# Performance work log

Hardware: AMD Instinct MI355X
Metric: run time of the kernel (lower is better)

The kernel has to match this reference:

```python
import jax, jax.numpy as jnp
import numpy as np
import math

B, S, D, H = 2, 2048, 1024, 16
DK = D // H
EPS = 1e-5


def setup_inputs() -> dict:
    key = jax.random.key(0)
    ks = jax.random.split(key, 16)
    s = 0.02
    inp = {
        "query": jax.random.normal(ks[0], (B, S, D), jnp.float32),
        "key": jax.random.normal(ks[1], (B, S, D), jnp.float32),
        "value": jax.random.normal(ks[2], (B, S, D), jnp.float32),
        "complexity": jax.random.uniform(ks[3], (B, S), jnp.float32),
        "mask": jnp.broadcast_to(jnp.tril(jnp.ones((S, S), bool))[None, None], (B, 1, S, S)),
        "wq": jax.random.normal(ks[4], (D, D), jnp.float32) * s,
        "bq": jnp.zeros((D,), jnp.float32),
        "wk": jax.random.normal(ks[5], (D, D), jnp.float32) * s,
        "bk": jnp.zeros((D,), jnp.float32),
        "wv": jax.random.normal(ks[6], (D, D), jnp.float32) * s,
        "bv": jnp.zeros((D,), jnp.float32),
        "wo": jax.random.normal(ks[7], (D, D), jnp.float32) * s,
        "bo": jnp.zeros((D,), jnp.float32),
        "ln_g": jnp.ones((D,), jnp.float32),
        "ln_b": jnp.zeros((D,), jnp.float32),
        "cpen": jnp.float32(1.0),
    }
    return inp


def reference(query, key, value, complexity, mask, wq, bq, wk, bk, wv, bv, wo, bo, ln_g, ln_b, cpen):
    # projections; torch Linear uses y = x @ W.T + b
    def proj(x, w, b):
        return (x @ w.T + b).reshape(B, S, H, DK).transpose(0, 2, 1, 3)  # [B,H,S,DK]

    Q = proj(query, wq, bq)
    K = proj(key, wk, bk)
    V = proj(value, wv, bv)

    scores = jnp.einsum("bhqd,bhkd->bhqk", Q, K) / math.sqrt(DK)
    # additive per-key-token complexity penalty broadcast over heads and queries
    scores = scores - cpen * complexity[:, None, None, :]
    scores = jnp.where(mask, scores, jnp.float32(-1e9))
    attn = jax.nn.softmax(scores, axis=-1)
    ctx = jnp.einsum("bhqk,bhkd->bhqd", attn, V)
    ctx = ctx.transpose(0, 2, 1, 3).reshape(B, S, D)
    out = ctx @ wo.T + bo
    x = out + query
    mu = jnp.mean(x, axis=-1, keepdims=True)
    var = jnp.mean(jnp.square(x - mu), axis=-1, keepdims=True)
    return (x - mu) * jax.lax.rsqrt(var + EPS) * ln_g + ln_b
```

## Files before the change

### kernel.cpp

```cpp
#include <hip/hip_runtime.h>

#define BB 2
#define SS 2048
#define DD 1024
#define HH 16
#define DKK 64
#define MROWS (BB*SS)
#define NEG_BIG (-30000.0f)

typedef unsigned short u16;
typedef unsigned int u32;
typedef __bf16 bf16x8 __attribute__((ext_vector_type(8)));
typedef float f32x4 __attribute__((ext_vector_type(4)));

__device__ __forceinline__ u16 f2bf(float f) {
    union { float f; u32 i; } w; w.f = f;
    u32 u = w.i;
    return (u16)((u + 0x7fffu + ((u >> 16) & 1u)) >> 16);
}
__device__ __forceinline__ float bf2f(u16 u) {
    union { u32 i; float f; } w; w.i = ((u32)u) << 16; return w.f;
}
__device__ __forceinline__ u32 pack2(float lo, float hi) {
    union { float f; u32 i; } a, b; a.f = lo; b.f = hi;
    return (a.i >> 16) | (b.i & 0xffff0000u);
}
__device__ __forceinline__ void gl2lds16(const u16* g, u16* l) {
    __builtin_amdgcn_global_load_lds(
        (const __attribute__((address_space(1))) void*)g,
        (__attribute__((address_space(3))) void*)l, 16, 0, 0);
}

__global__ __launch_bounds__(256)
void cvt_w(const float* __restrict__ w0, const float* __restrict__ w1,
           const float* __restrict__ w2, const float* __restrict__ w3,
           u16* __restrict__ dst)
{
    const float* srcs[4] = {w0, w1, w2, w3};
    const float* s = srcs[blockIdx.y];
    int i = (blockIdx.x * 256 + threadIdx.x) * 8;
    float4 a = *(const float4*)(s + i);
    float4 b = *(const float4*)(s + i + 4);
    uint4 o;
    o.x = pack2(a.x, a.y); o.y = pack2(a.z, a.w);
    o.z = pack2(b.x, b.y); o.w = pack2(b.z, b.w);
    *(uint4*)(dst + (size_t)blockIdx.y * DD * DD + i) = o;
}

__global__ __launch_bounds__(256)
void cvt_x(const float* __restrict__ s, u16* __restrict__ dst)
{
    int i = (blockIdx.x * 256 + threadIdx.x) * 8;
    float4 a = *(const float4*)(s + i);
    float4 b = *(const float4*)(s + i + 4);
    uint4 o;
    o.x = pack2(a.x, a.y); o.y = pack2(a.z, a.w);
    o.z = pack2(b.x, b.y); o.w = pack2(b.z, b.w);
    *(uint4*)(dst + i) = o;
}

__global__ __launch_bounds__(256)
void cvt_a3(const float* __restrict__ q, const float* __restrict__ k,
            const float* __restrict__ v, u16* __restrict__ qb,
            u16* __restrict__ kb, u16* __restrict__ vb)
{
    int y = blockIdx.y;
    const float* s = (y == 0) ? q : (y == 1) ? k : v;
    u16* d = (y == 0) ? qb : (y == 1) ? kb : vb;
    int i = (blockIdx.x * 256 + threadIdx.x) * 8;
    float4 a = *(const float4*)(s + i);
    float4 b = *(const float4*)(s + i + 4);
    uint4 o;
    o.x = pack2(a.x, a.y); o.y = pack2(a.z, a.w);
    o.z = pack2(b.x, b.y); o.w = pack2(b.z, b.w);
    *(uint4*)(d + i) = o;
}

__global__ __launch_bounds__(256, 2)
void qkv_gemm(const u16* __restrict__ qbf, const u16* __restrict__ kbf,
              const u16* __restrict__ vbf, const u16* __restrict__ wbf,
              const float* __restrict__ bq, const float* __restrict__ bk,
              const float* __restrict__ bv,
              u16* __restrict__ qh, u16* __restrict__ kh, u16* __restrict__ vt)
{
    __shared__ __align__(16) u16 smem[16384];
    u16* As = smem;
    u16* Bs = smem + 8192;
    const int K = 1024;
    int y = blockIdx.y;
    const u16* A = (y == 0) ? qbf : (y == 1) ? kbf : vbf;
    const u16* Wb = wbf + (size_t)y * DD * DD;
    const float* bias = (y == 0) ? bq : (y == 1) ? bk : bv;
    u16* out = (y == 0) ? qh : (y == 1) ? kh : vt;

    int tid  = threadIdx.x;
    int wave = tid >> 6, lane = tid & 63;
    int quad = lane >> 4, l16 = lane & 15;
    int bm = blockIdx.x >> 3;
    int bn = blockIdx.x & 7;
    int row0 = bm * 128, col0 = bn * 128;
    int wm = (wave >> 1) * 64, wn = (wave & 1) * 64;

    f32x4 acc[4][4] = {};

    for (int k0 = 0; k0 < K; k0 += 64) {
        __syncthreads();
        #pragma unroll
        for (int c = 0; c < 4; ++c) {
            int r0 = (c * 4 + wave) * 8;
            gl2lds16(A  + (size_t)(row0 + r0 + (lane >> 3)) * K + k0 + (lane & 7) * 8,
                     As + r0 * 64);
            gl2lds16(Wb + (size_t)(col0 + r0 + (lane >> 3)) * K + k0 + (lane & 7) * 8,
                     Bs + r0 * 64);
        }
        __syncthreads();
        #pragma unroll
        for (int kk = 0; kk < 2; ++kk) {
            bf16x8 af[4], bfv[4];
            #pragma unroll
            for (int i = 0; i < 4; ++i)
                af[i] = *(const bf16x8*)&As[(wm + i * 16 + l16) * 64 + kk * 32 + quad * 8];
            #pragma unroll
            for (int j = 0; j < 4; ++j)
                bfv[j] = *(const bf16x8*)&Bs[(wn + j * 16 + l16) * 64 + kk * 32 + quad * 8];
            #pragma unroll
            for (int i = 0; i < 4; ++i)
                #pragma unroll
                for (int j = 0; j < 4; ++j)
                    acc[i][j] = __builtin_amdgcn_mfma_f32_16x16x32_bf16(af[i], bfv[j], acc[i][j], 0, 0, 0);
        }
    }

    if (y == 2) {
        u16* Ct = smem;
        int b = row0 >> 11;
        int s0 = row0 & (SS - 1);
        #pragma unroll
        for (int p = 0; p < 2; ++p) {
            __syncthreads();
            if ((wave & 1) == p) {
                #pragma unroll
                for (int j = 0; j < 4; ++j) {
                    int dkl = j * 16 + l16;
                    float bvv = bias[col0 + p * 64 + dkl];
                    #pragma unroll
                    for (int i = 0; i < 4; ++i) {
                        uint2 pw;
                        pw.x = pack2(acc[i][j][0] + bvv, acc[i][j][1] + bvv);
                        pw.y = pack2(acc[i][j][2] + bvv, acc[i][j][3] + bvv);
                        *(uint2*)&Ct[dkl * 136 + wm + i * 16 + quad * 4] = pw;
                    }
                }
            }
            __syncthreads();
            int dkl = tid >> 2, seg = (tid & 3) * 32;
            int n = col0 + p * 64 + dkl;
            int h = n >> 6, dk = n & 63;
            u16* dst = out + (((size_t)(b * HH + h)) * DKK + dk) * SS + s0 + seg;
            #pragma unroll
            for (int u = 0; u < 4; ++u)
                *(uint4*)(dst + u * 8) = *(const uint4*)&Ct[dkl * 136 + seg + u * 8];
        }
        return;
    }

    #pragma unroll
    for (int j = 0; j < 4; ++j) {
        int n = col0 + wn + j * 16 + l16;
        float bvv = bias[n];
        #pragma unroll
        for (int i = 0; i < 4; ++i) {
            int rbase = row0 + wm + i * 16 + quad * 4;
            #pragma unroll
            for (int r = 0; r < 4; ++r) {
                int m = rbase + r;
                int b = m >> 11, s = m & (SS - 1);
                int h = n >> 6, dk = n & 63;
                out[(((size_t)(b * HH + h)) * SS + s) * DKK + dk] = f2bf(acc[i][j][r] + bvv);
            }
        }
    }
}

__global__ __launch_bounds__(256, 2)
void gemm_osk(const u16* __restrict__ A, const u16* __restrict__ Wb,
              const float* __restrict__ bias, float* __restrict__ P)
{
    __shared__ __align__(16) u16 smem[16384];
    u16* As = smem;
    u16* Bs = smem + 8192;
    const int K = 1024;
    int khalf = blockIdx.y;
    int tid  = threadIdx.x;
    int wave = tid >> 6, lane = tid & 63;
    int quad = lane >> 4, l16 = lane & 15;
    int bm = blockIdx.x >> 3;
    int bn = blockIdx.x & 7;
    int row0 = bm * 128, col0 = bn * 128;
    int wm = (wave >> 1) * 64, wn = (wave & 1) * 64;

    f32x4 acc[4][4] = {};

    for (int k0 = khalf * 512; k0 < khalf * 512 + 512; k0 += 64) {
        __syncthreads();
        #pragma unroll
        for (int c = 0; c < 4; ++c) {
            int r0 = (c * 4 + wave) * 8;
            gl2lds16(A  + (size_t)(row0 + r0 + (lane >> 3)) * K + k0 + (lane & 7) * 8,
                     As + r0 * 64);
            gl2lds16(Wb + (size_t)(col0 + r0 + (lane >> 3)) * K + k0 + (lane & 7) * 8,
                     Bs + r0 * 64);
        }
        __syncthreads();
        #pragma unroll
        for (int kk = 0; kk < 2; ++kk) {
            bf16x8 af[4], bfv[4];
            #pragma unroll
            for (int i = 0; i < 4; ++i)
                af[i] = *(const bf16x8*)&As[(wm + i * 16 + l16) * 64 + kk * 32 + quad * 8];
            #pragma unroll
            for (int j = 0; j < 4; ++j)
                bfv[j] = *(const bf16x8*)&Bs[(wn + j * 16 + l16) * 64 + kk * 32 + quad * 8];
            #pragma unroll
            for (int i = 0; i < 4; ++i)
                #pragma unroll
                for (int j = 0; j < 4; ++j)
                    acc[i][j] = __builtin_amdgcn_mfma_f32_16x16x32_bf16(af[i], bfv[j], acc[i][j], 0, 0, 0);
        }
    }

    float* Pd = P + (size_t)khalf * MROWS * DD;
    #pragma unroll
    for (int j = 0; j < 4; ++j) {
        int n = col0 + wn + j * 16 + l16;
        float bvv = (khalf == 0) ? bias[n] : 0.f;
        #pragma unroll
        for (int i = 0; i < 4; ++i) {
            int rbase = row0 + wm + i * 16 + quad * 4;
            #pragma unroll
            for (int r = 0; r < 4; ++r)
                Pd[(size_t)(rbase + r) * DD + n] = acc[i][j][r] + bvv;
        }
    }
}

template<int MODE>
__global__ __launch_bounds__(256, 2)
void gemm_nt(const u16* __restrict__ A, const u16* __restrict__ Wb,
             const float* __restrict__ bias, u16* __restrict__ out)
{
    __shared__ __align__(16) u16 smem[16384];
    u16* As = smem;
    u16* Bs = smem + 8192;
    const int K = 1024;
    int tid  = threadIdx.x;
    int wave = tid >> 6, lane = tid & 63;
    int quad = lane >> 4, l16 = lane & 15;
    int bm = blockIdx.x >> 3;
    int bn = blockIdx.x & 7;
    int row0 = bm * 128, col0 = bn * 128;
    int wm = (wave >> 1) * 64, wn = (wave & 1) * 64;

    f32x4 acc[4][4] = {};

    for (int k0 = 0; k0 < K; k0 += 64) {
        __syncthreads();
        #pragma unroll
        for (int c = 0; c < 4; ++c) {
            int r0 = (c * 4 + wave) * 8;
            gl2lds16(A  + (size_t)(row0 + r0 + (lane >> 3)) * K + k0 + (lane & 7) * 8,
                     As + r0 * 64);
            gl2lds16(Wb + (size_t)(col0 + r0 + (lane >> 3)) * K + k0 + (lane & 7) * 8,
                     Bs + r0 * 64);
        }
        __syncthreads();
        #pragma unroll
        for (int kk = 0; kk < 2; ++kk) {
            bf16x8 af[4], bfv[4];
            #pragma unroll
            for (int i = 0; i < 4; ++i)
                af[i] = *(const bf16x8*)&As[(wm + i * 16 + l16) * 64 + kk * 32 + quad * 8];
            #pragma unroll
            for (int j = 0; j < 4; ++j)
                bfv[j] = *(const bf16x8*)&Bs[(wn + j * 16 + l16) * 64 + kk * 32 + quad * 8];
            #pragma unroll
            for (int i = 0; i < 4; ++i)
                #pragma unroll
                for (int j = 0; j < 4; ++j)
                    acc[i][j] = __builtin_amdgcn_mfma_f32_16x16x32_bf16(af[i], bfv[j], acc[i][j], 0, 0, 0);
        }
    }

    if (MODE == 2) {
        u16* Ct = smem;
        int b = row0 >> 11;
        int s0 = row0 & (SS - 1);
        #pragma unroll
        for (int p = 0; p < 2; ++p) {
            __syncthreads();
            if ((wave & 1) == p) {
                #pragma unroll
                for (int j = 0; j < 4; ++j) {
                    int dkl = j * 16 + l16;
                    float bvv = bias[col0 + p * 64 + dkl];
                    #pragma unroll
                    for (int i = 0; i < 4; ++i) {
                        uint2 pw;
                        pw.x = pack2(acc[i][j][0] + bvv, acc[i][j][1] + bvv);
                        pw.y = pack2(acc[i][j][2] + bvv, acc[i][j][3] + bvv);
                        *(uint2*)&Ct[dkl * 136 + wm + i * 16 + quad * 4] = pw;
                    }
                }
            }
            __syncthreads();
            int dkl = tid >> 2, seg = (tid & 3) * 32;
            int n = col0 + p * 64 + dkl;
            int h = n >> 6, dk = n & 63;
            u16* dst = out + (((size_t)(b * HH + h)) * DKK + dk) * SS + s0 + seg;
            #pragma unroll
            for (int u = 0; u < 4; ++u)
                *(uint4*)(dst + u * 8) = *(const uint4*)&Ct[dkl * 136 + seg + u * 8];
        }
        return;
    }

    #pragma unroll
    for (int j = 0; j < 4; ++j) {
        int n = col0 + wn + j * 16 + l16;
        float bvv = bias[n];
        #pragma unroll
        for (int i = 0; i < 4; ++i) {
            int rbase = row0 + wm + i * 16 + quad * 4;
            #pragma unroll
            for (int r = 0; r < 4; ++r) {
                int m = rbase + r;
                float v = acc[i][j][r] + bvv;
                if (MODE == 0) {
                    int b = m >> 11, s = m & (SS - 1);
                    int h = n >> 6, dk = n & 63;
                    out[(((size_t)(b * HH + h)) * SS + s) * DKK + dk] = f2bf(v);
                } else {
                    out[(size_t)m * DD + n] = f2bf(v);
                }
            }
        }
    }
}

__global__ __launch_bounds__(256, 3)
void attn5(const u16* __restrict__ Qh, const u16* __restrict__ Kh,
           const u16* __restrict__ Vt, const float* __restrict__ comp,
           const float* __restrict__ cpen_p, u16* __restrict__ ctx)
{
    __shared__ __align__(16) u16 Kl[64 * 64];
    __shared__ __align__(16) u16 Vtl[64 * 64];
    __shared__ __align__(16) u16 Pb[4][16 * 72];

    int tid  = threadIdx.x;
    int wave = tid >> 6, lane = tid & 63;
    int quad = lane >> 4, l16 = lane & 15;
    int blk = blockIdx.x;
    int bh  = blk & 31;
    int qt  = 31 - (blk >> 5);
    int q0  = qt * 64;
    int b = bh >> 4, h = bh & 15;
    float cpen = cpen_p[0];

    const u16* Qb = Qh + (size_t)bh * SS * DKK;
    const u16* Kb = Kh + (size_t)bh * SS * DKK;
    const u16* Vb = Vt + (size_t)bh * DKK * SS;

    int myq = q0 + wave * 16 + l16;
    bf16x8 qf0 = *(const bf16x8*)&Qb[(size_t)myq * DKK + quad * 8];
    bf16x8 qf1 = *(const bf16x8*)&Qb[(size_t)myq * DKK + 32 + quad * 8];

    f32x4 o[4] = {};
    float m_i = NEG_BIG, l_i = 0.f;

    for (int kt = 0; kt <= qt; ++kt) {
        __syncthreads();
        if (wave < 2) {
            #pragma unroll
            for (int c = 0; c < 4; ++c) {
                int idx = wave * 4 + c;
                gl2lds16(Kb + (size_t)kt * 4096 + idx * 512 + lane * 8,
                         Kl + idx * 512);
            }
        } else {
            #pragma unroll
            for (int c = 0; c < 4; ++c) {
                int r0 = ((wave - 2) * 4 + c) * 8;
                gl2lds16(Vb + (size_t)(r0 + (lane >> 3)) * SS + kt * 64 + (lane & 7) * 8,
                         Vtl + r0 * 64);
            }
        }
        __syncthreads();

        f32x4 sc[4] = {};
        #pragma unroll
        for (int jj = 0; jj < 4; ++jj) {
            bf16x8 kf0 = *(const bf16x8*)&Kl[(jj * 16 + l16) * 64 + quad * 8];
            bf16x8 kf1 = *(const bf16x8*)&Kl[(jj * 16 + l16) * 64 + 32 + quad * 8];
            sc[jj] = __builtin_amdgcn_mfma_f32_16x16x32_bf16(kf0, qf0, sc[jj], 0, 0, 0);
            sc[jj] = __builtin_amdgcn_mfma_f32_16x16x32_bf16(kf1, qf1, sc[jj], 0, 0, 0);
        }
        bool diag = (kt == qt);
        #pragma unroll
        for (int jj = 0; jj < 4; ++jj) {
            f32x4 c4 = *(const f32x4*)&comp[b * SS + kt * 64 + jj * 16 + quad * 4];
            int kb0 = kt * 64 + jj * 16 + quad * 4;
            #pragma unroll
            for (int r = 0; r < 4; ++r) {
                float sv = sc[jj][r] * 0.125f - cpen * c4[r];
                if (diag && (kb0 + r > myq)) sv = NEG_BIG;
                sc[jj][r] = sv;
            }
        }
        float mx = NEG_BIG;
        #pragma unroll
        for (int jj = 0; jj < 4; ++jj)
            #pragma unroll
            for (int r = 0; r < 4; ++r) mx = fmaxf(mx, sc[jj][r]);
        mx = fmaxf(mx, __shfl_xor(mx, 16, 64));
        mx = fmaxf(mx, __shfl_xor(mx, 32, 64));
        float mnew = fmaxf(m_i, mx);
        float alpha = __expf(m_i - mnew);
        m_i = mnew;
        float ls = 0.f;
        #pragma unroll
        for (int jj = 0; jj < 4; ++jj)
            #pragma unroll
            for (int r = 0; r < 4; ++r) {
                float p = __expf(sc[jj][r] - mnew);
                sc[jj][r] = p;
                ls += p;
            }
        ls += __shfl_xor(ls, 16, 64);
        ls += __shfl_xor(ls, 32, 64);
        l_i = l_i * alpha + ls;
        #pragma unroll
        for (int jj = 0; jj < 4; ++jj)
            #pragma unroll
            for (int r = 0; r < 4; ++r) o[jj][r] *= alpha;

        #pragma unroll
        for (int jj = 0; jj < 4; ++jj) {
            uint2 pw;
            pw.x = pack2(sc[jj][0], sc[jj][1]);
            pw.y = pack2(sc[jj][2], sc[jj][3]);
            *(uint2*)&Pb[wave][l16 * 72 + jj * 16 + quad * 4] = pw;
        }
        #pragma unroll
        for (int kk = 0; kk < 2; ++kk) {
            bf16x8 pf = *(const bf16x8*)&Pb[wave][l16 * 72 + kk * 32 + quad * 8];
            #pragma unroll
            for (int jj = 0; jj < 4; ++jj) {
                bf16x8 vf = *(const bf16x8*)&Vtl[(jj * 16 + l16) * 64 + kk * 32 + quad * 8];
                o[jj] = __builtin_amdgcn_mfma_f32_16x16x32_bf16(vf, pf, o[jj], 0, 0, 0);
            }
        }
    }

    float inv = 1.f / l_i;
    #pragma unroll
    for (int jj = 0; jj < 4; ++jj) {
        uint2 ow;
        ow.x = pack2(o[jj][0] * inv, o[jj][1] * inv);
        ow.y = pack2(o[jj][2] * inv, o[jj][3] * inv);
        *(uint2*)&Pb[wave][l16 * 72 + jj * 16 + quad * 4] = ow;
    }
    int qq = lane >> 2;
    int dseg = (lane & 3) * 16;
    uint4 r0 = *(const uint4*)&Pb[wave][qq * 72 + dseg];
    uint4 r1 = *(const uint4*)&Pb[wave][qq * 72 + dseg + 8];
    u16* dst = ctx + ((size_t)(b * SS + q0 + wave * 16 + qq)) * DD + h * DKK + dseg;
    *(uint4*)dst = r0;
    *(uint4*)(dst + 8) = r1;
}

__global__ __launch_bounds__(256)
void ln_res(const u16* __restrict__ po, const float* __restrict__ query,
            const float* __restrict__ g, const float* __restrict__ bb,
            float* __restrict__ out)
{
    int row = blockIdx.x;
    int tid = threadIdx.x;
    int lane = tid & 63, wave = tid >> 6;
    size_t base = (size_t)row * DD + tid * 4;
    __align__(8) u16 tp[4];
    *(uint2*)tp = *(const uint2*)(po + base);
    float4 q4 = *(const float4*)(query + base);
    float x[4];
    x[0] = bf2f(tp[0]) + q4.x; x[1] = bf2f(tp[1]) + q4.y;
    x[2] = bf2f(tp[2]) + q4.z; x[3] = bf2f(tp[3]) + q4.w;
    float s1 = 0.f, s2 = 0.f;
    #pragma unroll
    for (int i = 0; i < 4; ++i) { s1 += x[i]; s2 += x[i] * x[i]; }
    #pragma unroll
    for (int off = 1; off < 64; off <<= 1) {
        s1 += __shfl_xor(s1, off, 64);
        s2 += __shfl_xor(s2, off, 64);
    }
    __shared__ float red1[4], red2[4];
    if (lane == 0) { red1[wave] = s1; red2[wave] = s2; }
    __syncthreads();
    float t1 = red1[0] + red1[1] + red1[2] + red1[3];
    float t2 = red2[0] + red2[1] + red2[2] + red2[3];
    float mean = t1 * (1.f / 1024.f);
    float var  = fmaxf(t2 * (1.f / 1024.f) - mean * mean, 0.f);
    float rstd = rsqrtf(var + 1e-5f);
    float4 g4 = *(const float4*)(g + tid * 4);
    float4 b4 = *(const float4*)(bb + tid * 4);
    float4 ov;
    ov.x = (x[0] - mean) * rstd * g4.x + b4.x;
    ov.y = (x[1] - mean) * rstd * g4.y + b4.y;
    ov.z = (x[2] - mean) * rstd * g4.z + b4.z;
    ov.w = (x[3] - mean) * rstd * g4.w + b4.w;
    *(float4*)(out + base) = ov;
}

__global__ __launch_bounds__(256)
void ln_res2(const float* __restrict__ p0, const float* __restrict__ p1,
             const float* __restrict__ query, const float* __restrict__ g,
             const float* __restrict__ bb, float* __restrict__ out)
{
    int row = blockIdx.x;
    int tid = threadIdx.x;
    int lane = tid & 63, wave = tid >> 6;
    size_t base = (size_t)row * DD + tid * 4;
    float4 a4 = *(const float4*)(p0 + base);
    float4 c4 = *(const float4*)(p1 + base);
    float4 q4 = *(const float4*)(query + base);
    float x[4];
    x[0] = a4.x + c4.x + q4.x; x[1] = a4.y + c4.y + q4.y;
    x[2] = a4.z + c4.z + q4.z; x[3] = a4.w + c4.w + q4.w;
    float s1 = 0.f, s2 = 0.f;
    #pragma unroll
    for (int i = 0; i < 4; ++i) { s1 += x[i]; s2 += x[i] * x[i]; }
    #pragma unroll
    for (int off = 1; off < 64; off <<= 1) {
        s1 += __shfl_xor(s1, off, 64);
        s2 += __shfl_xor(s2, off, 64);
    }
    __shared__ float red1[4], red2[4];
    if (lane == 0) { red1[wave] = s1; red2[wave] = s2; }
    __syncthreads();
    float t1 = red1[0] + red1[1] + red1[2] + red1[3];
    float t2 = red2[0] + red2[1] + red2[2] + red2[3];
    float mean = t1 * (1.f / 1024.f);
    float var  = fmaxf(t2 * (1.f / 1024.f) - mean * mean, 0.f);
    float rstd = rsqrtf(var + 1e-5f);
    float4 g4 = *(const float4*)(g + tid * 4);
    float4 b4 = *(const float4*)(bb + tid * 4);
    float4 ov;
    ov.x = (x[0] - mean) * rstd * g4.x + b4.x;
    ov.y = (x[1] - mean) * rstd * g4.y + b4.y;
    ov.z = (x[2] - mean) * rstd * g4.z + b4.z;
    ov.w = (x[3] - mean) * rstd * g4.w + b4.w;
    *(float4*)(out + base) = ov;
}

extern "C" void kernel_launch(void* const* d_in, const int* in_sizes, int n_in,
                              void* d_out, int out_size, void* d_ws, size_t ws_size,
                              hipStream_t stream)
{
    const float* query = (const float*)d_in[0];
    const float* key   = (const float*)d_in[1];
    const float* value = (const float*)d_in[2];
    const float* comp  = (const float*)d_in[3];
    const float* wq = (const float*)d_in[5];
    const float* bq = (const float*)d_in[6];
    const float* wk = (const float*)d_in[7];
    const float* bk = (const float*)d_in[8];
    const float* wv = (const float*)d_in[9];
    const float* bv = (const float*)d_in[10];
    const float* wo = (const float*)d_in[11];
    const float* bo = (const float*)d_in[12];
    const float* lng = (const float*)d_in[13];
    const float* lnb = (const float*)d_in[14];
    const float* cpen = (const float*)d_in[15];
    float* outp = (float*)d_out;

    const size_t NE = (size_t)MROWS * DD;
    const size_t WE = (size_t)DD * DD;
    u16* wbf = (u16*)d_out;
    u16* cxr = wbf + 4 * WE;

    cvt_w<<<dim3(512, 4), 256, 0, stream>>>(wq, wk, wv, wo, wbf);

    if (ws_size >= (size_t)48 * 1024 * 1024) {
        u16* qbf = (u16*)d_ws;
        u16* kbf = qbf + NE;
        u16* vbf = kbf + NE;
        u16* qh  = vbf + NE;
        u16* kh  = qh + NE;
        u16* vt  = kh + NE;
        float* P0 = (float*)d_ws;
        float* P1 = (float*)(qbf + 2 * NE);

        cvt_a3<<<dim3(2048, 3), 256, 0, stream>>>(query, key, value, qbf, kbf, vbf);
        qkv_gemm<<<dim3(256, 3), 256, 0, stream>>>(qbf, kbf, vbf, wbf,
                                                   bq, bk, bv, qh, kh, vt);
        attn5<<<1024, 256, 0, stream>>>(qh, kh, vt, comp, cpen, cxr);
        gemm_osk<<<dim3(256, 2), 256, 0, stream>>>(cxr, wbf + 3 * WE, bo, P0);
        ln_res2<<<MROWS, 256, 0, stream>>>(P0, P1, query, lng, lnb, outp);
    } else {
        u16* qh = (u16*)d_ws;
        u16* kh = qh + NE;
        u16* vt = kh + NE;
        u16* po = kh;

        cvt_x<<<2048, 256, 0, stream>>>(query, cxr);
        gemm_nt<0><<<256, 256, 0, stream>>>(cxr, wbf + 0 * WE, bq, qh);
        cvt_x<<<2048, 256, 0, stream>>>(key, cxr);
        gemm_nt<0><<<256, 256, 0, stream>>>(cxr, wbf + 1 * WE, bk, kh);
        cvt_x<<<2048, 256, 0, stream>>>(value, cxr);
        gemm_nt<2><<<256, 256, 0, stream>>>(cxr, wbf + 2 * WE, bv, vt);
        attn5<<<1024, 256, 0, stream>>>(qh, kh, vt, comp, cpen, cxr);
        gemm_nt<1><<<256, 256, 0, stream>>>(cxr, wbf + 3 * WE, bo, po);
        ln_res<<<MROWS, 256, 0, stream>>>(po, query, lng, lnb, outp);
    }
}
```

Measured before the change: 277.9 us.

## Fuse fp32-to-bf16 activation conversion into QKV GEMM and XOR-swizzle LDS tiles

Result: faster. 271.8 us (-2.2%).

```diff
diff --git a/kernel.cpp b/kernel.cpp
--- a/kernel.cpp
+++ b/kernel.cpp
@@ -59,26 +59,9 @@
     *(uint4*)(dst + i) = o;
 }
 
-__global__ __launch_bounds__(256)
-void cvt_a3(const float* __restrict__ q, const float* __restrict__ k,
-            const float* __restrict__ v, u16* __restrict__ qb,
-            u16* __restrict__ kb, u16* __restrict__ vb)
-{
-    int y = blockIdx.y;
-    const float* s = (y == 0) ? q : (y == 1) ? k : v;
-    u16* d = (y == 0) ? qb : (y == 1) ? kb : vb;
-    int i = (blockIdx.x * 256 + threadIdx.x) * 8;
-    float4 a = *(const float4*)(s + i);
-    float4 b = *(const float4*)(s + i + 4);
-    uint4 o;
-    o.x = pack2(a.x, a.y); o.y = pack2(a.z, a.w);
-    o.z = pack2(b.x, b.y); o.w = pack2(b.z, b.w);
-    *(uint4*)(d + i) = o;
-}
-
 __global__ __launch_bounds__(256, 2)
-void qkv_gemm(const u16* __restrict__ qbf, const u16* __restrict__ kbf,
-              const u16* __restrict__ vbf, const u16* __restrict__ wbf,
+void qkv_gemm(const float* __restrict__ qf, const float* __restrict__ kf,
+              const float* __restrict__ vf, const u16* __restrict__ wbf,
               const float* __restrict__ bq, const float* __restrict__ bk,
               const float* __restrict__ bv,
               u16* __restrict__ qh, u16* __restrict__ kh, u16* __restrict__ vt)
@@ -88,7 +71,7 @@
     u16* Bs = smem + 8192;
     const int K = 1024;
     int y = blockIdx.y;
-    const u16* A = (y == 0) ? qbf : (y == 1) ? kbf : vbf;
+    const float* A = (y == 0) ? qf : (y == 1) ? kf : vf;
     const u16* Wb = wbf + (size_t)y * DD * DD;
     const float* bias = (y == 0) ? bq : (y == 1) ? bk : bv;
     u16* out = (y == 0) ? qh : (y == 1) ? kh : vt;
@@ -101,16 +84,31 @@
     int row0 = bm * 128, col0 = bn * 128;
     int wm = (wave >> 1) * 64, wn = (wave & 1) * 64;
 
+    int srow = tid >> 3;
+    int scol = (tid & 7) * 8;
+    int swz  = ((tid & 7) ^ ((tid >> 3) & 7)) * 8;
+    int bswz = ((lane & 7) ^ ((lane >> 3) & 7)) * 8;
+
     f32x4 acc[4][4] = {};
 
     for (int k0 = 0; k0 < K; k0 += 64) {
-        __syncthreads();
+        uint4 av[4];
+        #pragma unroll
+        for (int c = 0; c < 4; ++c) {
+            const float* ap = A + (size_t)(row0 + srow + c * 32) * K + k0 + scol;
+            float4 lo = *(const float4*)ap;
+            float4 hi = *(const float4*)(ap + 4);
+            av[c].x = pack2(lo.x, lo.y); av[c].y = pack2(lo.z, lo.w);
+            av[c].z = pack2(hi.x, hi.y); av[c].w = pack2(hi.z, hi.w);
+        }
+        __syncthreads();
+        #pragma unroll
+        for (int c = 0; c < 4; ++c)
+            *(uint4*)&As[(srow + c * 32) * 64 + swz] = av[c];
         #pragma unroll
         for (int c = 0; c < 4; ++c) {
             int r0 = (c * 4 + wave) * 8;
-            gl2lds16(A  + (size_t)(row0 + r0 + (lane >> 3)) * K + k0 + (lane & 7) * 8,
-                     As + r0 * 64);
-            gl2lds16(Wb + (size_t)(col0 + r0 + (lane >> 3)) * K + k0 + (lane & 7) * 8,
+            gl2lds16(Wb + (size_t)(col0 + r0 + (lane >> 3)) * K + k0 + bswz,
                      Bs + r0 * 64);
         }
         __syncthreads();
@@ -119,10 +117,12 @@
             bf16x8 af[4], bfv[4];
             #pragma unroll
             for (int i = 0; i < 4; ++i)
-                af[i] = *(const bf16x8*)&As[(wm + i * 16 + l16) * 64 + kk * 32 + quad * 8];
+                af[i] = *(const bf16x8*)&As[(wm + i * 16 + l16) * 64 +
+                                            (((kk * 4 + quad) ^ (l16 & 7)) * 8)];
             #pragma unroll
             for (int j = 0; j < 4; ++j)
-                bfv[j] = *(const bf16x8*)&Bs[(wn + j * 16 + l16) * 64 + kk * 32 + quad * 8];
+                bfv[j] = *(const bf16x8*)&Bs[(wn + j * 16 + l16) * 64 +
+                                             (((kk * 4 + quad) ^ (l16 & 7)) * 8)];
             #pragma unroll
             for (int i = 0; i < 4; ++i)
                 #pragma unroll
@@ -198,6 +198,7 @@
     int bn = blockIdx.x & 7;
     int row0 = bm * 128, col0 = bn * 128;
     int wm = (wave >> 1) * 64, wn = (wave & 1) * 64;
+    int bswz = ((lane & 7) ^ ((lane >> 3) & 7)) * 8;
 
     f32x4 acc[4][4] = {};
 
@@ -206,9 +207,9 @@
         #pragma unroll
         for (int c = 0; c < 4; ++c) {
             int r0 = (c * 4 + wave) * 8;
-            gl2lds16(A  + (size_t)(row0 + r0 + (lane >> 3)) * K + k0 + (lane & 7) * 8,
+            gl2lds16(A  + (size_t)(row0 + r0 + (lane >> 3)) * K + k0 + bswz,
                      As + r0 * 64);
-            gl2lds16(Wb + (size_t)(col0 + r0 + (lane >> 3)) * K + k0 + (lane & 7) * 8,
+            gl2lds16(Wb + (size_t)(col0 + r0 + (lane >> 3)) * K + k0 + bswz,
                      Bs + r0 * 64);
         }
         __syncthreads();
@@ -217,10 +218,12 @@
             bf16x8 af[4], bfv[4];
             #pragma unroll
             for (int i = 0; i < 4; ++i)
-                af[i] = *(const bf16x8*)&As[(wm + i * 16 + l16) * 64 + kk * 32 + quad * 8];
+                af[i] = *(const bf16x8*)&As[(wm + i * 16 + l16) * 64 +
+                                            (((kk * 4 + quad) ^ (l16 & 7)) * 8)];
             #pragma unroll
             for (int j = 0; j < 4; ++j)
-                bfv[j] = *(const bf16x8*)&Bs[(wn + j * 16 + l16) * 64 + kk * 32 + quad * 8];
+                bfv[j] = *(const bf16x8*)&Bs[(wn + j * 16 + l16) * 64 +
+                                             (((kk * 4 + quad) ^ (l16 & 7)) * 8)];
             #pragma unroll
             for (int i = 0; i < 4; ++i)
                 #pragma unroll
@@ -348,7 +351,7 @@
 }
 
 __global__ __launch_bounds__(256, 3)
-void attn5(const u16* __restrict__ Qh, const u16* __restrict__ Kh,
+void attn6(const u16* __restrict__ Qh, const u16* __restrict__ Kh,
            const u16* __restrict__ Vt, const float* __restrict__ comp,
            const float* __restrict__ cpen_p, u16* __restrict__ ctx)
 {
@@ -365,6 +368,7 @@
     int q0  = qt * 64;
     int b = bh >> 4, h = bh & 15;
     float cpen = cpen_p[0];
+    int lswz = ((lane & 7) ^ ((lane >> 3) & 7)) * 8;
 
     const u16* Qb = Qh + (size_t)bh * SS * DKK;
     const u16* Kb = Kh + (size_t)bh * SS * DKK;
@@ -383,14 +387,14 @@
             #pragma unroll
             for (int c = 0; c < 4; ++c) {
                 int idx = wave * 4 + c;
-                gl2lds16(Kb + (size_t)kt * 4096 + idx * 512 + lane * 8,
+                gl2lds16(Kb + (size_t)kt * 4096 + idx * 512 + (lane >> 3) * 64 + lswz,
                          Kl + idx * 512);
             }
         } else {
             #pragma unroll
             for (int c = 0; c < 4; ++c) {
                 int r0 = ((wave - 2) * 4 + c) * 8;
-                gl2lds16(Vb + (size_t)(r0 + (lane >> 3)) * SS + kt * 64 + (lane & 7) * 8,
+                gl2lds16(Vb + (size_t)(r0 + (lane >> 3)) * SS + kt * 64 + lswz,
                          Vtl + r0 * 64);
             }
         }
@@ -399,8 +403,8 @@
         f32x4 sc[4] = {};
         #pragma unroll
         for (int jj = 0; jj < 4; ++jj) {
-            bf16x8 kf0 = *(const bf16x8*)&Kl[(jj * 16 + l16) * 64 + quad * 8];
-            bf16x8 kf1 = *(const bf16x8*)&Kl[(jj * 16 + l16) * 64 + 32 + quad * 8];
+            bf16x8 kf0 = *(const bf16x8*)&Kl[(jj * 16 + l16) * 64 + ((quad ^ (l16 & 7)) * 8)];
+            bf16x8 kf1 = *(const bf16x8*)&Kl[(jj * 16 + l16) * 64 + (((4 + quad) ^ (l16 & 7)) * 8)];
             sc[jj] = __builtin_amdgcn_mfma_f32_16x16x32_bf16(kf0, qf0, sc[jj], 0, 0, 0);
             sc[jj] = __builtin_amdgcn_mfma_f32_16x16x32_bf16(kf1, qf1, sc[jj], 0, 0, 0);
         }
@@ -455,8 +459,9 @@
             bf16x8 pf = *(const bf16x8*)&Pb[wave][l16 * 72 + kk * 32 + quad * 8];
             #pragma unroll
             for (int jj = 0; jj < 4; ++jj) {
-                bf16x8 vf = *(const bf16x8*)&Vtl[(jj * 16 + l16) * 64 + kk * 32 + quad * 8];
-                o[jj] = __builtin_amdgcn_mfma_f32_16x16x32_bf16(vf, pf, o[jj], 0, 0, 0);
+                bf16x8 vfr = *(const bf16x8*)&Vtl[(jj * 16 + l16) * 64 +
+                                                  (((kk * 4 + quad) ^ (l16 & 7)) * 8)];
+                o[jj] = __builtin_amdgcn_mfma_f32_16x16x32_bf16(vfr, pf, o[jj], 0, 0, 0);
             }
         }
     }
@@ -588,20 +593,16 @@
 
     cvt_w<<<dim3(512, 4), 256, 0, stream>>>(wq, wk, wv, wo, wbf);
 
-    if (ws_size >= (size_t)48 * 1024 * 1024) {
-        u16* qbf = (u16*)d_ws;
-        u16* kbf = qbf + NE;
-        u16* vbf = kbf + NE;
-        u16* qh  = vbf + NE;
-        u16* kh  = qh + NE;
-        u16* vt  = kh + NE;
+    if (ws_size >= (size_t)32 * 1024 * 1024) {
+        u16* qh = (u16*)d_ws;
+        u16* kh = qh + NE;
+        u16* vt = kh + NE;
         float* P0 = (float*)d_ws;
-        float* P1 = (float*)(qbf + 2 * NE);
-
-        cvt_a3<<<dim3(2048, 3), 256, 0, stream>>>(query, key, value, qbf, kbf, vbf);
-        qkv_gemm<<<dim3(256, 3), 256, 0, stream>>>(qbf, kbf, vbf, wbf,
+        float* P1 = P0 + NE;
+
+        qkv_gemm<<<dim3(256, 3), 256, 0, stream>>>(query, key, value, wbf,
                                                    bq, bk, bv, qh, kh, vt);
-        attn5<<<1024, 256, 0, stream>>>(qh, kh, vt, comp, cpen, cxr);
+        attn6<<<1024, 256, 0, stream>>>(qh, kh, vt, comp, cpen, cxr);
         gemm_osk<<<dim3(256, 2), 256, 0, stream>>>(cxr, wbf + 3 * WE, bo, P0);
         ln_res2<<<MROWS, 256, 0, stream>>>(P0, P1, query, lng, lnb, outp);
     } else {
@@ -616,7 +617,7 @@
         gemm_nt<0><<<256, 256, 0, stream>>>(cxr, wbf + 1 * WE, bk, kh);
         cvt_x<<<2048, 256, 0, stream>>>(value, cxr);
         gemm_nt<2><<<256, 256, 0, stream>>>(cxr, wbf + 2 * WE, bv, vt);
-        attn5<<<1024, 256, 0, stream>>>(qh, kh, vt, comp, cpen, cxr);
+        attn6<<<1024, 256, 0, stream>>>(qh, kh, vt, comp, cpen, cxr);
         gemm_nt<1><<<256, 256, 0, stream>>>(cxr, wbf + 3 * WE, bo, po);
         ln_res<<<MROWS, 256, 0, stream>>>(po, query, lng, lnb, outp);
     }
```
